# Optimization experiments

Measured on AMD Instinct MI355X. Metric: run time of the kernel, lower is better.

## Reference

```python
import jax, jax.numpy as jnp
import numpy as np

EPS = 1e-12  # torch F.normalize eps


def setup_inputs() -> dict:
    key = jax.random.key(0)
    ks = jax.random.split(key, 6)
    B, N, P, H = 32, 512, 8, 300
    node_attr = jax.random.normal(ks[0], (B, N, P, H), dtype=jnp.float32)
    edge_attr = jax.random.normal(ks[1], (B, 1, 1, H), dtype=jnp.float32)  # unused for ins_id=0
    instruction = jax.random.normal(ks[2], (B, H), dtype=jnp.float32)
    distribution = jax.random.uniform(ks[3], (B, N), dtype=jnp.float32)  # unused for ins_id=0
    node_prop_similarities = jax.random.uniform(ks[4], (B, P), dtype=jnp.float32)
    node_mask = jnp.zeros((B, N), dtype=jnp.float32)
    # weight_node_properties initialized as stacked identities; perturb to be nontrivial
    W_node = jnp.tile(jnp.eye(H, dtype=jnp.float32)[None], (P, 1, 1)) \
        + 0.02 * jax.random.normal(ks[5], (P, H, H), dtype=jnp.float32)
    w_state = jnp.ones((H,), dtype=jnp.float32)  # weight_state_score init = ones
    return {
        "node_attr": node_attr,
        "edge_attr": edge_attr,
        "instruction": instruction,
        "distribution": distribution,
        "ins_id": 0,
        "node_prop_similarities": node_prop_similarities,
        "node_mask": node_mask,
        "W_node": W_node,
        "w_state": w_state,
    }


def reference(node_attr, edge_attr, instruction, distribution, ins_id,
              node_prop_similarities, node_mask, W_node, w_state):
    # n_ins=3, ins_id=0 branch of NSMCell.forward
    # node_attr: (B,N,P,H) -> (B,P,N,H)
    x = jnp.transpose(node_attr, (0, 2, 1, 3))
    # broadcast-multiply instruction, then per-property matmul with W_node[p]
    y = instruction[:, None, None, :] * x                      # (B,P,N,H)
    z = jnp.einsum('bpnh,phk->bpnk', y, W_node)                # (B,P,N,H)
    z = z * node_prop_similarities[:, :, None, None]           # weight by property similarity
    # torch F.normalize default dim=1 -> L2-normalize over the P axis
    norm = jnp.sqrt(jnp.sum(z * z, axis=1, keepdims=True))
    z = z / jnp.maximum(norm, EPS)
    s = jnp.sum(z, axis=1)                                     # (B,N,H) sum over P
    node_scores = jax.nn.elu(s)                                # dropout p=0 -> identity
    scores = jnp.einsum('bnh,h->bn', node_scores, w_state)     # (B,N)
    return jax.nn.softmax(scores + node_mask, axis=1)
```

## Files before the change

### kernel.cpp

```cpp
#include <hip/hip_runtime.h>

#define B 32
#define N 512
#define P 8
#define H 300
#define HP 320
#define EPSN 1e-12f
#define NT 32
#define SA_STRIDE 328

typedef __attribute__((ext_vector_type(8))) short bf16x8;
typedef __attribute__((ext_vector_type(4))) float f32x4;

__device__ __forceinline__ unsigned short f2bf(float f) {
    unsigned int u = __float_as_uint(f);
    u += 0x7FFFu + ((u >> 16) & 1u);
    return (unsigned short)(u >> 16);
}
__device__ __forceinline__ float bf2f(unsigned short h) {
    return __uint_as_float(((unsigned int)h) << 16);
}

__global__ __launch_bounds__(256)
void nsm_prep_w(const float* __restrict__ W,
                unsigned short* __restrict__ whi,
                unsigned short* __restrict__ wlo)
{
    const int gid  = blockIdx.x * 256 + threadIdx.x;
    const int fb   = gid >> 6;
    const int lane = gid & 63;
    const int p  = fb / 200;
    const int rm = fb % 200;
    const int ht = rm / 20;
    const int kt = rm % 20;
    const int k  = kt * 16 + (lane & 15);
    const int h0 = ht * 32 + (lane >> 4) * 8;

    bf16x8 hv, lv;
    #pragma unroll
    for (int j = 0; j < 8; ++j) {
        int h = h0 + j;
        float wv = (h < H && k < H) ? W[((size_t)p * H + h) * H + k] : 0.f;
        unsigned short hb = f2bf(wv);
        hv[j] = (short)hb;
        lv[j] = (short)f2bf(wv - bf2f(hb));
    }
    size_t off = (size_t)fb * 512 + (size_t)lane * 8;
    *(bf16x8*)(whi + off) = hv;
    *(bf16x8*)(wlo + off) = lv;
}

__global__ __launch_bounds__(256, 2)
void nsm_scores_mfma(const float* __restrict__ node_attr,
                     const float* __restrict__ instruction,
                     const float* __restrict__ nps,
                     const unsigned short* __restrict__ whi,
                     const unsigned short* __restrict__ wlo,
                     const float* __restrict__ w_state,
                     float* __restrict__ scores)
{
    __shared__ unsigned short sAh[NT * SA_STRIDE];
    __shared__ unsigned short sAl[NT * SA_STRIDE];
    __shared__ float sI[HP];

    const int t  = threadIdx.x;
    const int b  = blockIdx.y;
    const int n0 = blockIdx.x * NT;
    const int w  = t >> 6;
    const int l  = t & 63;

    for (int idx = t; idx < HP; idx += 256)
        sI[idx] = (idx < H) ? instruction[b * H + idx] : 0.f;

    f32x4 S1[2][5], S2[2][5];
    #pragma unroll
    for (int nt = 0; nt < 2; ++nt)
        #pragma unroll
        for (int kt = 0; kt < 5; ++kt) {
            S1[nt][kt] = (f32x4){0.f, 0.f, 0.f, 0.f};
            S2[nt][kt] = (f32x4){0.f, 0.f, 0.f, 0.f};
        }

    const int r  = t >> 3;
    const int cs = t & 7;

    for (int p = 0; p < P; ++p) {
        __syncthreads();

        const float* srcA = node_attr + ((size_t)((b * N + n0 + r) * P + p)) * H;
        unsigned short* dh = &sAh[r * SA_STRIDE];
        unsigned short* dl = &sAl[r * SA_STRIDE];
        #pragma unroll
        for (int i = 0; i < 10; ++i) {
            int s = cs + i * 8;
            int h = s * 4;
            float4 v = make_float4(0.f, 0.f, 0.f, 0.f);
            if (s < 75) {
                v = *(const float4*)(srcA + h);
                float4 sc = *(const float4*)&sI[h];
                v.x *= sc.x; v.y *= sc.y; v.z *= sc.z; v.w *= sc.w;
            }
            unsigned short h0b = f2bf(v.x), h1b = f2bf(v.y);
            unsigned short h2b = f2bf(v.z), h3b = f2bf(v.w);
            unsigned short l0b = f2bf(v.x - bf2f(h0b)), l1b = f2bf(v.y - bf2f(h1b));
            unsigned short l2b = f2bf(v.z - bf2f(h2b)), l3b = f2bf(v.w - bf2f(h3b));
            *(uint2*)(dh + h) = make_uint2((unsigned)h0b | ((unsigned)h1b << 16),
                                           (unsigned)h2b | ((unsigned)h3b << 16));
            *(uint2*)(dl + h) = make_uint2((unsigned)l0b | ((unsigned)l1b << 16),
                                           (unsigned)l2b | ((unsigned)l3b << 16));
        }
        __syncthreads();

        f32x4 acc[2][5];
        #pragma unroll
        for (int nt = 0; nt < 2; ++nt)
            #pragma unroll
            for (int kt = 0; kt < 5; ++kt)
                acc[nt][kt] = (f32x4){0.f, 0.f, 0.f, 0.f};

        for (int ht = 0; ht < 10; ++ht) {
            bf16x8 ah[2], al[2];
            const int hoff = ht * 32 + (l >> 4) * 8;
            #pragma unroll
            for (int nt = 0; nt < 2; ++nt) {
                const int row = nt * 16 + (l & 15);
                ah[nt] = *(const bf16x8*)&sAh[row * SA_STRIDE + hoff];
                al[nt] = *(const bf16x8*)&sAl[row * SA_STRIDE + hoff];
            }
            #pragma unroll
            for (int kt = 0; kt < 5; ++kt) {
                size_t off = ((size_t)(p * 10 + ht) * 20 + (w * 5 + kt)) * 512
                           + (size_t)l * 8;
                bf16x8 bh = *(const bf16x8*)(whi + off);
                bf16x8 bl = *(const bf16x8*)(wlo + off);
                #pragma unroll
                for (int nt = 0; nt < 2; ++nt) {
                    acc[nt][kt] = __builtin_amdgcn_mfma_f32_16x16x32_bf16(ah[nt], bh, acc[nt][kt], 0, 0, 0);
                    acc[nt][kt] = __builtin_amdgcn_mfma_f32_16x16x32_bf16(al[nt], bh, acc[nt][kt], 0, 0, 0);
                    acc[nt][kt] = __builtin_amdgcn_mfma_f32_16x16x32_bf16(ah[nt], bl, acc[nt][kt], 0, 0, 0);
                }
            }
        }

        const float sim = nps[b * P + p];
        #pragma unroll
        for (int nt = 0; nt < 2; ++nt)
            #pragma unroll
            for (int kt = 0; kt < 5; ++kt) {
                f32x4 z = acc[nt][kt] * sim;
                S1[nt][kt] += z;
                S2[nt][kt] += z * z;
            }
    }

    #pragma unroll
    for (int nt = 0; nt < 2; ++nt) {
        #pragma unroll
        for (int j = 0; j < 4; ++j) {
            float part = 0.f;
            #pragma unroll
            for (int kt = 0; kt < 5; ++kt) {
                int k = w * 80 + kt * 16 + (l & 15);
                if (k < H) {
                    float s1 = S1[nt][kt][j];
                    float s2 = S2[nt][kt][j];
                    float denom = fmaxf(sqrtf(s2), EPSN);
                    float v = s1 / denom;
                    float e = v > 0.f ? v : expm1f(v);
                    part += e * w_state[k];
                }
            }
            part += __shfl_xor(part, 1, 16);
            part += __shfl_xor(part, 2, 16);
            part += __shfl_xor(part, 4, 16);
            part += __shfl_xor(part, 8, 16);
            if ((l & 15) == 0)
                atomicAdd(&scores[b * N + n0 + nt * 16 + (l >> 4) * 4 + j], part);
        }
    }
}

__global__ __launch_bounds__(256)
void nsm_softmax_kernel(float* __restrict__ out, const float* __restrict__ mask)
{
    __shared__ float redm[4];
    __shared__ float reds[4];
    const int b = blockIdx.x;
    const int t = threadIdx.x;

    float v0 = out[b * N + t]       + mask[b * N + t];
    float v1 = out[b * N + 256 + t] + mask[b * N + 256 + t];

    float m = fmaxf(v0, v1);
    m = fmaxf(m, __shfl_xor(m, 1, 64));
    m = fmaxf(m, __shfl_xor(m, 2, 64));
    m = fmaxf(m, __shfl_xor(m, 4, 64));
    m = fmaxf(m, __shfl_xor(m, 8, 64));
    m = fmaxf(m, __shfl_xor(m, 16, 64));
    m = fmaxf(m, __shfl_xor(m, 32, 64));
    const int wave = t >> 6;
    const int lane = t & 63;
    if (lane == 0) redm[wave] = m;
    __syncthreads();
    m = fmaxf(fmaxf(redm[0], redm[1]), fmaxf(redm[2], redm[3]));

    float e0 = expf(v0 - m);
    float e1 = expf(v1 - m);
    float s = e0 + e1;
    s += __shfl_xor(s, 1, 64);
    s += __shfl_xor(s, 2, 64);
    s += __shfl_xor(s, 4, 64);
    s += __shfl_xor(s, 8, 64);
    s += __shfl_xor(s, 16, 64);
    s += __shfl_xor(s, 32, 64);
    if (lane == 0) reds[wave] = s;
    __syncthreads();
    s = reds[0] + reds[1] + reds[2] + reds[3];

    out[b * N + t]       = e0 / s;
    out[b * N + 256 + t] = e1 / s;
}

extern "C" void kernel_launch(void* const* d_in, const int* in_sizes, int n_in,
                              void* d_out, int out_size, void* d_ws, size_t ws_size,
                              hipStream_t stream)
{
    const float* node_attr   = (const float*)d_in[0];
    const float* instruction = (const float*)d_in[2];
    const float* nps         = (const float*)d_in[5];
    const float* node_mask   = (const float*)d_in[6];
    const float* W_node      = (const float*)d_in[7];
    const float* w_state     = (const float*)d_in[8];
    float* out = (float*)d_out;

    unsigned short* whi = (unsigned short*)d_ws;
    unsigned short* wlo = whi + 1600 * 512;

    nsm_prep_w<<<dim3(400), 256, 0, stream>>>(W_node, whi, wlo);

    (void)hipMemsetAsync(out, 0, (size_t)B * N * sizeof(float), stream);

    dim3 grid(N / NT, B);
    nsm_scores_mfma<<<grid, 256, 0, stream>>>(node_attr, instruction, nps,
                                              whi, wlo, w_state, out);
    nsm_softmax_kernel<<<dim3(B), 256, 0, stream>>>(out, node_mask);
}
```

Measured before the change: 376.7 us.

## Switch to single fp16 MFMA and prepack A fragments in separate kernel

Replaces the split bf16 hi/lo emulation (three MFMAs per tile) with a single fp16 MFMA per tile, cutting matrix work by about three times and halving weight fragment traffic. Adds a prep kernel that scales node_attr by the instruction, converts it to fp16 and writes it to global memory in MFMA fragment layout. The main kernel then reads fragments straight from global memory with no shared memory or barriers. The cost is an extra global round trip for activations, about 40MB of fp16 written and read back, plus lower precision: fp16 has a 10-bit mantissa versus roughly 16 bits for the bf16 pair, and values outside fp16 range would overflow.

```diff
diff --git a/kernel.cpp b/kernel.cpp
--- a/kernel.cpp
+++ b/kernel.cpp
@@ -7,24 +7,14 @@
 #define HP 320
 #define EPSN 1e-12f
 #define NT 32
-#define SA_STRIDE 328
-
-typedef __attribute__((ext_vector_type(8))) short bf16x8;
-typedef __attribute__((ext_vector_type(4))) float f32x4;
-
-__device__ __forceinline__ unsigned short f2bf(float f) {
-    unsigned int u = __float_as_uint(f);
-    u += 0x7FFFu + ((u >> 16) & 1u);
-    return (unsigned short)(u >> 16);
-}
-__device__ __forceinline__ float bf2f(unsigned short h) {
-    return __uint_as_float(((unsigned int)h) << 16);
-}
+#define NB (N / NT)
+#define SAP 328
+
+typedef _Float16 f16x8 __attribute__((ext_vector_type(8)));
+typedef float f32x4 __attribute__((ext_vector_type(4)));
 
 __global__ __launch_bounds__(256)
-void nsm_prep_w(const float* __restrict__ W,
-                unsigned short* __restrict__ whi,
-                unsigned short* __restrict__ wlo)
+void nsm_prep_w(const float* __restrict__ W, _Float16* __restrict__ wfrag)
 {
     const int gid  = blockIdx.x * 256 + threadIdx.x;
     const int fb   = gid >> 6;
@@ -36,41 +26,81 @@
     const int k  = kt * 16 + (lane & 15);
     const int h0 = ht * 32 + (lane >> 4) * 8;
 
-    bf16x8 hv, lv;
+    f16x8 v;
     #pragma unroll
     for (int j = 0; j < 8; ++j) {
         int h = h0 + j;
         float wv = (h < H && k < H) ? W[((size_t)p * H + h) * H + k] : 0.f;
-        unsigned short hb = f2bf(wv);
-        hv[j] = (short)hb;
-        lv[j] = (short)f2bf(wv - bf2f(hb));
-    }
-    size_t off = (size_t)fb * 512 + (size_t)lane * 8;
-    *(bf16x8*)(whi + off) = hv;
-    *(bf16x8*)(wlo + off) = lv;
+        v[j] = (_Float16)wv;
+    }
+    *(f16x8*)(wfrag + (size_t)fb * 512 + (size_t)lane * 8) = v;
+}
+
+__global__ __launch_bounds__(256)
+void nsm_prep_a(const float* __restrict__ node_attr,
+                const float* __restrict__ instruction,
+                _Float16* __restrict__ afrag)
+{
+    __shared__ _Float16 sA[NT * SAP];
+
+    const int t  = threadIdx.x;
+    const int nb = blockIdx.x;
+    const int b  = blockIdx.y;
+    const int p  = blockIdx.z;
+    const int r  = t >> 3;
+    const int cs = t & 7;
+
+    const float* srcA = node_attr + ((size_t)((b * N + nb * NT + r) * P + p)) * H;
+    const float* ins  = instruction + (size_t)b * H;
+
+    #pragma unroll
+    for (int i = 0; i < 10; ++i) {
+        int s = cs + i * 8;
+        int h = s * 4;
+        _Float16 o0 = (_Float16)0.f, o1 = o0, o2 = o0, o3 = o0;
+        if (s < 75) {
+            float4 v  = *(const float4*)(srcA + h);
+            float4 sc = *(const float4*)(ins + h);
+            o0 = (_Float16)(v.x * sc.x);
+            o1 = (_Float16)(v.y * sc.y);
+            o2 = (_Float16)(v.z * sc.z);
+            o3 = (_Float16)(v.w * sc.w);
+        }
+        sA[r * SAP + h]     = o0;
+        sA[r * SAP + h + 1] = o1;
+        sA[r * SAP + h + 2] = o2;
+        sA[r * SAP + h + 3] = o3;
+    }
+    __syncthreads();
+
+    const int w = t >> 6;
+    const int l = t & 63;
+    const size_t unit_base = ((size_t)(b * NB + nb) * P + p) * 20;
+    #pragma unroll
+    for (int uu = 0; uu < 5; ++uu) {
+        int u  = w + uu * 4;
+        int ht = u >> 1;
+        int nt = u & 1;
+        f16x8 v = *(const f16x8*)&sA[(nt * 16 + (l & 15)) * SAP + ht * 32 + (l >> 4) * 8];
+        *(f16x8*)(afrag + (unit_base + u) * 512 + (size_t)l * 8) = v;
+    }
 }
 
 __global__ __launch_bounds__(256, 2)
-void nsm_scores_mfma(const float* __restrict__ node_attr,
-                     const float* __restrict__ instruction,
+void nsm_scores_mfma(const _Float16* __restrict__ afrag,
+                     const _Float16* __restrict__ wfrag,
                      const float* __restrict__ nps,
-                     const unsigned short* __restrict__ whi,
-                     const unsigned short* __restrict__ wlo,
                      const float* __restrict__ w_state,
                      float* __restrict__ scores)
 {
-    __shared__ unsigned short sAh[NT * SA_STRIDE];
-    __shared__ unsigned short sAl[NT * SA_STRIDE];
-    __shared__ float sI[HP];
-
     const int t  = threadIdx.x;
+    const int nb = blockIdx.x;
     const int b  = blockIdx.y;
-    const int n0 = blockIdx.x * NT;
     const int w  = t >> 6;
     const int l  = t & 63;
 
-    for (int idx = t; idx < HP; idx += 256)
-        sI[idx] = (idx < H) ? instruction[b * H + idx] : 0.f;
+    const _Float16* Ab = afrag + ((size_t)(b * NB + nb) * P) * 10240 + (size_t)l * 8;
+    const _Float16* Wb = wfrag + (size_t)(w * 5) * 512 + (size_t)l * 8;
 
     f32x4 S1[2][5], S2[2][5];
     #pragma unroll
@@ -81,35 +111,9 @@
             S2[nt][kt] = (f32x4){0.f, 0.f, 0.f, 0.f};
         }
 
-    const int r  = t >> 3;
-    const int cs = t & 7;
-
     for (int p = 0; p < P; ++p) {
-        __syncthreads();
-
-        const float* srcA = node_attr + ((size_t)((b * N + n0 + r) * P + p)) * H;
-        unsigned short* dh = &sAh[r * SA_STRIDE];
-        unsigned short* dl = &sAl[r * SA_STRIDE];
-        #pragma unroll
-        for (int i = 0; i < 10; ++i) {
-            int s = cs + i * 8;
-            int h = s * 4;
-            float4 v = make_float4(0.f, 0.f, 0.f, 0.f);
-            if (s < 75) {
-                v = *(const float4*)(srcA + h);
-                float4 sc = *(const float4*)&sI[h];
-                v.x *= sc.x; v.y *= sc.y; v.z *= sc.z; v.w *= sc.w;
-            }
-            unsigned short h0b = f2bf(v.x), h1b = f2bf(v.y);
-            unsigned short h2b = f2bf(v.z), h3b = f2bf(v.w);
-            unsigned short l0b = f2bf(v.x - bf2f(h0b)), l1b = f2bf(v.y - bf2f(h1b));
-            unsigned short l2b = f2bf(v.z - bf2f(h2b)), l3b = f2bf(v.w - bf2f(h3b));
-            *(uint2*)(dh + h) = make_uint2((unsigned)h0b | ((unsigned)h1b << 16),
-                                           (unsigned)h2b | ((unsigned)h3b << 16));
-            *(uint2*)(dl + h) = make_uint2((unsigned)l0b | ((unsigned)l1b << 16),
-                                           (unsigned)l2b | ((unsigned)l3b << 16));
-        }
-        __syncthreads();
+        const _Float16* Ap = Ab + (size_t)p * 10240;
+        const _Float16* Wp = Wb + (size_t)p * 102400;
 
         f32x4 acc[2][5];
         #pragma unroll
@@ -118,27 +122,15 @@
             for (int kt = 0; kt < 5; ++kt)
                 acc[nt][kt] = (f32x4){0.f, 0.f, 0.f, 0.f};
 
+        #pragma unroll
         for (int ht = 0; ht < 10; ++ht) {
-            bf16x8 ah[2], al[2];
-            const int hoff = ht * 32 + (l >> 4) * 8;
-            #pragma unroll
-            for (int nt = 0; nt < 2; ++nt) {
-                const int row = nt * 16 + (l & 15);
-                ah[nt] = *(const bf16x8*)&sAh[row * SA_STRIDE + hoff];
-                al[nt] = *(const bf16x8*)&sAl[row * SA_STRIDE + hoff];
-            }
+            f16x8 a0 = *(const f16x8*)(Ap + ht * 1024);
+            f16x8 a1 = *(const f16x8*)(Ap + ht * 1024 + 512);
             #pragma unroll
             for (int kt = 0; kt < 5; ++kt) {
-                size_t off = ((size_t)(p * 10 + ht) * 20 + (w * 5 + kt)) * 512
-                           + (size_t)l * 8;
-                bf16x8 bh = *(const bf16x8*)(whi + off);
-                bf16x8 bl = *(const bf16x8*)(wlo + off);
-                #pragma unroll
-                for (int nt = 0; nt < 2; ++nt) {
-                    acc[nt][kt] = __builtin_amdgcn_mfma_f32_16x16x32_bf16(ah[nt], bh, acc[nt][kt], 0, 0, 0);
-                    acc[nt][kt] = __builtin_amdgcn_mfma_f32_16x16x32_bf16(al[nt], bh, acc[nt][kt], 0, 0, 0);
-                    acc[nt][kt] = __builtin_amdgcn_mfma_f32_16x16x32_bf16(ah[nt], bl, acc[nt][kt], 0, 0, 0);
-                }
+                f16x8 wf = *(const f16x8*)(Wp + ht * 10240 + kt * 512);
+                acc[0][kt] = __builtin_amdgcn_mfma_f32_16x16x32_f16(a0, wf, acc[0][kt], 0, 0, 0);
+                acc[1][kt] = __builtin_amdgcn_mfma_f32_16x16x32_f16(a1, wf, acc[1][kt], 0, 0, 0);
             }
         }
 
@@ -175,7 +167,7 @@
             part += __shfl_xor(part, 4, 16);
             part += __shfl_xor(part, 8, 16);
             if ((l & 15) == 0)
-                atomicAdd(&scores[b * N + n0 + nt * 16 + (l >> 4) * 4 + j], part);
+                atomicAdd(&scores[b * N + nb * NT + nt * 16 + (l >> 4) * 4 + j], part);
         }
     }
 }
@@ -233,15 +225,15 @@
     const float* w_state     = (const float*)d_in[8];
     float* out = (float*)d_out;
 
-    unsigned short* whi = (unsigned short*)d_ws;
-    unsigned short* wlo = whi + 1600 * 512;
-
-    nsm_prep_w<<<dim3(400), 256, 0, stream>>>(W_node, whi, wlo);
+    _Float16* afrag = (_Float16*)d_ws;
+    _Float16* wfrag = afrag + (size_t)B * NB * P * 20 * 512;
+
+    nsm_prep_w<<<dim3(400), 256, 0, stream>>>(W_node, wfrag);
+    nsm_prep_a<<<dim3(NB, B, P), 256, 0, stream>>>(node_attr, instruction, afrag);
 
     (void)hipMemsetAsync(out, 0, (size_t)B * N * sizeof(float), stream);
 
-    dim3 grid(N / NT, B);
-    nsm_scores_mfma<<<grid, 256, 0, stream>>>(node_attr, instruction, nps,
-                                              whi, wlo, w_state, out);
+    dim3 grid(NB, B);
+    nsm_scores_mfma<<<grid, 256, 0, stream>>>(afrag, wfrag, nps, w_state, out);
     nsm_softmax_kernel<<<dim3(B), 256, 0, stream>>>(out, node_mask);
 }
```

Measured after the change: 335.2 us. -11.0%, faster.
